# Kernel tuning notes

Hardware: AMD Instinct MI355X
Metric: run time of the kernel (lower is better)

## Reference

```python
import jax, jax.numpy as jnp
import numpy as np

DIM = 256

def setup_inputs() -> dict:
    key = jax.random.key(0)
    k1, k2 = jax.random.split(key)
    X = jax.random.normal(k1, (4, 4096, DIM), dtype=jnp.float32)
    # fused QKV projection weight, stored as (dim, 3*dim) so y = X @ W + b
    W = jax.random.normal(k2, (DIM, 3 * DIM), dtype=jnp.float32) * (1.0 / np.sqrt(DIM))
    b = jnp.zeros((3 * DIM,), dtype=jnp.float32)
    return {"X": X, "W": W, "b": b}

def reference(X, W, b):
    dim = X.shape[-1]
    QKV = X @ W + b                      # [B, S, 3*dim]
    Q, K, V = jnp.split(QKV, 3, axis=-1)  # each [B, S, dim]
    scores = jnp.einsum('bqd,bkd->bqk', Q, K) / jnp.sqrt(jnp.float32(dim))
    weights = jax.nn.softmax(scores, axis=-1)  # [B, S, S]
    return jnp.einsum('bqk,bkd->bqd', weights, V)
```

## Files before the change

kernel.cpp:

```cpp
#include <hip/hip_runtime.h>
#include <hip/hip_bf16.h>
#include <hip/hip_fp16.h>

#define DIMD 256
#define SLEN 4096
#define KT 32

typedef __attribute__((ext_vector_type(8))) short short8;
typedef __attribute__((ext_vector_type(4))) short bf16x4;
typedef __attribute__((ext_vector_type(4))) float f32x4;
typedef unsigned int u32;

__device__ __forceinline__ ushort f2bf(float x) {
  union { float f; unsigned u; } v; v.f = x;
  unsigned r = v.u + 0x7fffu + ((v.u >> 16) & 1u);
  return (ushort)(r >> 16);
}

typedef __attribute__((address_space(1))) const u32 g_u32;
typedef __attribute__((address_space(3))) u32 l_u32;
__device__ __forceinline__ void gld_lds16(const void* g, void* l) {
  __builtin_amdgcn_global_load_lds((g_u32*)g, (l_u32*)l, 16, 0, 0);
}

__global__ __launch_bounds__(256) void wt_prep(const float* __restrict__ W,
                                               ushort* __restrict__ Wt) {
  __shared__ float T[32][257];
  const int t = threadIdx.x;
  const int n0 = blockIdx.x * 32;
#pragma unroll
  for (int pass = 0; pass < 8; ++pass) {
    const int k = pass * 32 + (t >> 3);
    const int c4 = (t & 7) * 4;
    const float4 f = *(const float4*)&W[(size_t)k * 768 + n0 + c4];
    T[c4 + 0][k] = f.x; T[c4 + 1][k] = f.y; T[c4 + 2][k] = f.z; T[c4 + 3][k] = f.w;
  }
  __syncthreads();
  const int n = t >> 3, kb = (t & 7) * 32;
#pragma unroll
  for (int j8 = 0; j8 < 4; ++j8) {
    short8 o;
#pragma unroll
    for (int j = 0; j < 8; ++j) o[j] = (short)f2bf(T[n][kb + j8 * 8 + j]);
    *(short8*)&Wt[(size_t)(n0 + n) * 256 + kb + j8 * 8] = o;
  }
}

__global__ __launch_bounds__(256, 2) void qkv_proj(const float* __restrict__ X,
                                                   const ushort* __restrict__ Wt,
                                                   const float* __restrict__ bias,
                                                   ushort* __restrict__ Qo,
                                                   ushort* __restrict__ Ko,
                                                   ushort* __restrict__ Vto) {
  __shared__ ushort Xs[128 * 36];
  __shared__ ushort Ws[256 * 36];
  const int tid = threadIdx.x;
  const int w = tid >> 6, lane = tid & 63;
  const int qa = lane & 15, hi = lane >> 4;
  const int m0 = blockIdx.x * 128;
  const int seg = blockIdx.y;
  const int n0 = seg * 256;

  f32x4 acc[2][16];
#pragma unroll
  for (int t = 0; t < 2; ++t)
#pragma unroll
    for (int dc = 0; dc < 16; ++dc) acc[t][dc] = (f32x4){0.f, 0.f, 0.f, 0.f};

  for (int k0 = 0; k0 < 256; k0 += 32) {
    __syncthreads();
#pragma unroll
    for (int pass = 0; pass < 4; ++pass) {
      const int row = pass * 32 + (tid >> 3);
      const int c = tid & 7;
      const float4 f = *(const float4*)&X[(size_t)(m0 + row) * 256 + k0 + c * 4];
      bf16x4 h = {(short)f2bf(f.x), (short)f2bf(f.y), (short)f2bf(f.z), (short)f2bf(f.w)};
      *(bf16x4*)&Xs[row * 36 + c * 4] = h;
    }
#pragma unroll
    for (int pass = 0; pass < 4; ++pass) {
      const int n = pass * 64 + (tid >> 2);
      const int c = (tid & 3) * 8;
      short8 v = *(const short8*)&Wt[(size_t)(n0 + n) * 256 + k0 + c];
      *(short8*)&Ws[n * 36 + c] = v;
    }
    __syncthreads();
    const short8 xf0 = *(const short8*)&Xs[(w * 32 + qa) * 36 + hi * 8];
    const short8 xf1 = *(const short8*)&Xs[(w * 32 + 16 + qa) * 36 + hi * 8];
    __builtin_amdgcn_s_setprio(1);
#pragma unroll
    for (int dc = 0; dc < 16; ++dc) {
      const short8 wf = *(const short8*)&Ws[(dc * 16 + qa) * 36 + hi * 8];
      acc[0][dc] = __builtin_amdgcn_mfma_f32_16x16x32_bf16(xf0, wf, acc[0][dc], 0, 0, 0);
      acc[1][dc] = __builtin_amdgcn_mfma_f32_16x16x32_bf16(xf1, wf, acc[1][dc], 0, 0, 0);
    }
    __builtin_amdgcn_s_setprio(0);
  }

  const float sc = (seg == 0) ? 0.0625f : 1.0f;
#pragma unroll
  for (int dc = 0; dc < 16; ++dc) {
    const int nn = dc * 16 + qa;
    const float bv = bias[n0 + nn];
#pragma unroll
    for (int t = 0; t < 2; ++t) {
#pragma unroll
      for (int r = 0; r < 4; ++r) {
        const int m = m0 + w * 32 + t * 16 + hi * 4 + r;
        const ushort h = f2bf((acc[t][dc][r] + bv) * sc);
        if (seg == 0)      Qo[(size_t)m * 256 + nn] = h;
        else if (seg == 1) Ko[(size_t)m * 256 + nn] = h;
        else {
          const int bi = m >> 12, s = m & 4095;
          const int sp = (s & ~31) | ((s & 3) | (((s >> 4) & 1) << 2) | (((s >> 2) & 3) << 3));
          Vto[((size_t)bi * 256 + nn) * 4096 + sp] = h;
        }
      }
    }
  }
}

__device__ __forceinline__ void stage_kv(ushort* KsB, ushort* VsB,
                                         const ushort* Kb, const ushort* Vtb,
                                         int kv0, int w, int lane) {
#pragma unroll
  for (int it = 0; it < 2; ++it) {
    const int row = w * 4 + it * 2 + (lane >> 5);
    const int cb = (lane & 31) * 16;
    const char* src = (const char*)Kb + (size_t)(kv0 + row) * 512 + (cb ^ ((row & 7) << 4));
    gld_lds16(src, (char*)KsB + w * 2048 + it * 1024);
  }
#pragma unroll
  for (int it = 0; it < 2; ++it) {
    const int d = w * 32 + it * 16 + (lane >> 2);
    const int cb = (lane & 3) * 16;
    const char* src = (const char*)Vtb + (size_t)d * 8192 + (size_t)kv0 * 2 + (cb ^ ((d & 3) << 4));
    gld_lds16(src, (char*)VsB + w * 2048 + it * 1024);
  }
}

__global__ __launch_bounds__(512, 2) void flash_attn(const ushort* __restrict__ Q,
                                                     const ushort* __restrict__ K,
                                                     const ushort* __restrict__ Vt,
                                                     float* __restrict__ Out,
                                                     __half* __restrict__ Op,
                                                     float* __restrict__ Mp,
                                                     int nsplit, int kvn) {
  __shared__ __attribute__((aligned(16))) ushort Ks[3][KT * DIMD];
  __shared__ __attribute__((aligned(16))) ushort Vs[3][DIMD * KT];

  const int tid = threadIdx.x;
  const int w = tid >> 6, lane = tid & 63;
  const int nwg = gridDim.x;
  const int wg = (blockIdx.x & 7) * (nwg >> 3) + (blockIdx.x >> 3);
  const int split = wg >> 6;
  const int rest = wg & 63;
  const int b = rest >> 4;
  const int q0 = (rest & 15) * 256;
  const int qa = lane & 15, hi = lane >> 4;

  const ushort* Qr0 = Q + (size_t)(b * SLEN + q0 + w * 32 + qa) * DIMD;
  short8 qf0[8], qf1[8];
#pragma unroll
  for (int dc = 0; dc < 8; ++dc) {
    qf0[dc] = *(const short8*)(Qr0 + dc * 32 + hi * 8);
    qf1[dc] = *(const short8*)(Qr0 + 16 * DIMD + dc * 32 + hi * 8);
  }

  const f32x4 zero = {0.f, 0.f, 0.f, 0.f};
  f32x4 acc[2][16];
#pragma unroll
  for (int t = 0; t < 2; ++t)
#pragma unroll
    for (int dc = 0; dc < 16; ++dc) acc[t][dc] = zero;
  float mold0 = -1e30f, lrun0 = 0.f, mold1 = -1e30f, lrun1 = 0.f;
  short8 af0, af1;
  f32x4 sa0, sa1, sb0, sb1;

  const ushort* Kb = K + (size_t)b * SLEN * DIMD;
  const ushort* Vtb = Vt + (size_t)b * DIMD * SLEN;
  const int kv_begin = split * kvn;
  const int nt = kvn / KT;

  auto QK = [&](const char* KsB) {
    sa0 = zero; sa1 = zero; sb0 = zero; sb1 = zero;
    __builtin_amdgcn_s_setprio(1);
#pragma unroll
    for (int dc = 0; dc < 8; ++dc) {
      const int cb = dc * 64 + hi * 16;
      const short8 kf0 = *(const short8*)(KsB + ((qa * 512 + cb) ^ ((qa & 7) << 4)));
      const short8 kf1 = *(const short8*)(KsB + (((qa + 16) * 512 + cb) ^ ((qa & 7) << 4)));
      sa0 = __builtin_amdgcn_mfma_f32_16x16x32_bf16(kf0, qf0[dc], sa0, 0, 0, 0);
      sa1 = __builtin_amdgcn_mfma_f32_16x16x32_bf16(kf1, qf0[dc], sa1, 0, 0, 0);
      sb0 = __builtin_amdgcn_mfma_f32_16x16x32_bf16(kf0, qf1[dc], sb0, 0, 0, 0);
      sb1 = __builtin_amdgcn_mfma_f32_16x16x32_bf16(kf1, qf1[dc], sb1, 0, 0, 0);
    }
    __builtin_amdgcn_s_setprio(0);
  };

  auto FUSED = [&](const char* VsB, const char* KsB) {
    sa0 = zero; sa1 = zero; sb0 = zero; sb1 = zero;
    __builtin_amdgcn_s_setprio(1);
#pragma unroll
    for (int j = 0; j < 8; ++j) {
      const int d0 = (2 * j) * 16 + qa;
      const short8 vfa = *(const short8*)(VsB + d0 * 64 + ((hi * 16) ^ ((d0 & 3) << 4)));
      acc[0][2 * j] = __builtin_amdgcn_mfma_f32_16x16x32_bf16(af0, vfa, acc[0][2 * j], 0, 0, 0);
      acc[1][2 * j] = __builtin_amdgcn_mfma_f32_16x16x32_bf16(af1, vfa, acc[1][2 * j], 0, 0, 0);
      const int d1 = d0 + 16;
      const short8 vfb = *(const short8*)(VsB + d1 * 64 + ((hi * 16) ^ ((d1 & 3) << 4)));
      acc[0][2 * j + 1] = __builtin_amdgcn_mfma_f32_16x16x32_bf16(af0, vfb, acc[0][2 * j + 1], 0, 0, 0);
      acc[1][2 * j + 1] = __builtin_amdgcn_mfma_f32_16x16x32_bf16(af1, vfb, acc[1][2 * j + 1], 0, 0, 0);
      const int cb = j * 64 + hi * 16;
      const short8 kf0 = *(const short8*)(KsB + ((qa * 512 + cb) ^ ((qa & 7) << 4)));
      const short8 kf1 = *(const short8*)(KsB + (((qa + 16) * 512 + cb) ^ ((qa & 7) << 4)));
      sa0 = __builtin_amdgcn_mfma_f32_16x16x32_bf16(kf0, qf0[j], sa0, 0, 0, 0);
      sa1 = __builtin_amdgcn_mfma_f32_16x16x32_bf16(kf1, qf0[j], sa1, 0, 0, 0);
      sb0 = __builtin_amdgcn_mfma_f32_16x16x32_bf16(kf0, qf1[j], sb0, 0, 0, 0);
      sb1 = __builtin_amdgcn_mfma_f32_16x16x32_bf16(kf1, qf1[j], sb1, 0, 0, 0);
    }
    __builtin_amdgcn_s_setprio(0);
  };

  auto SM = [&]() {
    float m8a = fmaxf(fmaxf(fmaxf(sa0[0], sa0[1]), fmaxf(sa0[2], sa0[3])),
                      fmaxf(fmaxf(sa1[0], sa1[1]), fmaxf(sa1[2], sa1[3])));
    float m8b = fmaxf(fmaxf(fmaxf(sb0[0], sb0[1]), fmaxf(sb0[2], sb0[3])),
                      fmaxf(fmaxf(sb1[0], sb1[1]), fmaxf(sb1[2], sb1[3])));
    if (!__all(fmaxf(m8a - mold0, m8b - mold1) <= 4.0f)) {
      m8a = fmaxf(m8a, __shfl_xor(m8a, 16)); m8a = fmaxf(m8a, __shfl_xor(m8a, 32));
      m8b = fmaxf(m8b, __shfl_xor(m8b, 16)); m8b = fmaxf(m8b, __shfl_xor(m8b, 32));
      const float mn0 = fmaxf(mold0, m8a), fr0 = __expf(mold0 - mn0);
      const float mn1 = fmaxf(mold1, m8b), fr1 = __expf(mold1 - mn1);
      mold0 = mn0; lrun0 *= fr0; mold1 = mn1; lrun1 *= fr1;
      float fA[4], fB[4];
#pragma unroll
      for (int r = 0; r < 4; ++r) { fA[r] = __shfl(fr0, hi * 4 + r); fB[r] = __shfl(fr1, hi * 4 + r); }
#pragma unroll
      for (int dc = 0; dc < 16; ++dc)
#pragma unroll
        for (int r = 0; r < 4; ++r) { acc[0][dc][r] *= fA[r]; acc[1][dc][r] *= fB[r]; }
    }
    float ls0 = 0.f, ls1 = 0.f;
#pragma unroll
    for (int r = 0; r < 4; ++r) {
      float p = __expf(sa0[r] - mold0); ls0 += p; af0[r] = (short)f2bf(p);
      p = __expf(sa1[r] - mold0); ls0 += p; af0[4 + r] = (short)f2bf(p);
      p = __expf(sb0[r] - mold1); ls1 += p; af1[r] = (short)f2bf(p);
      p = __expf(sb1[r] - mold1); ls1 += p; af1[4 + r] = (short)f2bf(p);
    }
    lrun0 += ls0;
    lrun1 += ls1;
  };

  auto PV = [&](const char* VsB) {
    __builtin_amdgcn_s_setprio(1);
#pragma unroll
    for (int dc = 0; dc < 16; ++dc) {
      const int d = dc * 16 + qa;
      const short8 vf = *(const short8*)(VsB + d * 64 + ((hi * 16) ^ ((d & 3) << 4)));
      acc[0][dc] = __builtin_amdgcn_mfma_f32_16x16x32_bf16(af0, vf, acc[0][dc], 0, 0, 0);
      acc[1][dc] = __builtin_amdgcn_mfma_f32_16x16x32_bf16(af1, vf, acc[1][dc], 0, 0, 0);
    }
    __builtin_amdgcn_s_setprio(0);
  };

  stage_kv(Ks[0], Vs[0], Kb, Vtb, kv_begin, w, lane);
  stage_kv(Ks[1], Vs[1], Kb, Vtb, kv_begin + KT, w, lane);
  asm volatile("s_waitcnt vmcnt(0)" ::: "memory");
  __builtin_amdgcn_s_barrier();
  __builtin_amdgcn_sched_barrier(0);
  QK((const char*)Ks[0]);
  SM();

  int cur = 0;
  for (int it = 0; it < nt - 2; ++it) {
    const int nb = (cur == 0) ? 2 : cur - 1;
    stage_kv(Ks[nb], Vs[nb], Kb, Vtb, kv_begin + (it + 2) * KT, w, lane);
    __builtin_amdgcn_sched_barrier(0);
    asm volatile("s_waitcnt vmcnt(4)" ::: "memory");
    __builtin_amdgcn_sched_barrier(0);
    const int nx = (cur == 2) ? 0 : cur + 1;
    FUSED((const char*)Vs[cur], (const char*)Ks[nx]);
    SM();
    __builtin_amdgcn_s_barrier();
    __builtin_amdgcn_sched_barrier(0);
    cur = nx;
  }
  asm volatile("s_waitcnt vmcnt(0)" ::: "memory");
  __builtin_amdgcn_s_barrier();
  __builtin_amdgcn_sched_barrier(0);
  {
    const int nx = (cur == 2) ? 0 : cur + 1;
    FUSED((const char*)Vs[cur], (const char*)Ks[nx]);
    SM();
    PV((const char*)Vs[nx]);
  }

  lrun0 += __shfl_xor(lrun0, 16); lrun0 += __shfl_xor(lrun0, 32);
  lrun1 += __shfl_xor(lrun1, 16); lrun1 += __shfl_xor(lrun1, 32);
  float inv0[4], inv1[4];
#pragma unroll
  for (int r = 0; r < 4; ++r) {
    inv0[r] = 1.f / __shfl(lrun0, hi * 4 + r);
    inv1[r] = 1.f / __shfl(lrun1, hi * 4 + r);
  }
  if (nsplit == 1) {
    float* Ob = Out + (size_t)(b * SLEN + q0 + w * 32) * DIMD;
#pragma unroll
    for (int dc = 0; dc < 16; ++dc)
#pragma unroll
      for (int r = 0; r < 4; ++r) {
        Ob[(size_t)(hi * 4 + r) * DIMD + dc * 16 + qa] = acc[0][dc][r] * inv0[r];
        Ob[(size_t)(16 + hi * 4 + r) * DIMD + dc * 16 + qa] = acc[1][dc][r] * inv1[r];
      }
  } else {
    const size_t qrow0 = (size_t)b * SLEN + q0 + w * 32;
#pragma unroll
    for (int dc = 0; dc < 16; ++dc)
#pragma unroll
      for (int r = 0; r < 4; ++r) {
        Op[((qrow0 + hi * 4 + r) * nsplit + split) * DIMD + dc * 16 + qa] =
            __float2half(acc[0][dc][r] * inv0[r]);
        Op[((qrow0 + 16 + hi * 4 + r) * nsplit + split) * DIMD + dc * 16 + qa] =
            __float2half(acc[1][dc][r] * inv1[r]);
      }
    if (hi == 0) {
      Mp[(qrow0 + qa) * nsplit + split] = mold0 + __logf(lrun0);
      Mp[(qrow0 + 16 + qa) * nsplit + split] = mold1 + __logf(lrun1);
    }
  }
}

__global__ __launch_bounds__(256) void attn_merge(const __half* __restrict__ Op,
                                                  const float* __restrict__ Mp,
                                                  float* __restrict__ Out, int nsplit) {
  const int q = blockIdx.x, d = threadIdx.x;
  float Mx = -1e30f;
  for (int i = 0; i < nsplit; ++i) Mx = fmaxf(Mx, Mp[(size_t)q * nsplit + i]);
  float Wsum = 0.f, o = 0.f;
  for (int i = 0; i < nsplit; ++i) {
    const float wgt = __expf(Mp[(size_t)q * nsplit + i] - Mx);
    Wsum += wgt;
    o += wgt * __half2float(Op[((size_t)q * nsplit + i) * DIMD + d]);
  }
  Out[(size_t)q * DIMD + d] = o / Wsum;
}

extern "C" void kernel_launch(void* const* d_in, const int* in_sizes, int n_in,
                              void* d_out, int out_size, void* d_ws, size_t ws_size,
                              hipStream_t stream) {
  const float* X = (const float*)d_in[0];
  const float* W = (const float*)d_in[1];
  const float* bias = (const float*)d_in[2];
  char* wsb = (char*)d_ws;
  ushort* qw = (ushort*)wsb;
  ushort* kw = qw + (size_t)16384 * 256;
  ushort* vtw = kw + (size_t)16384 * 256;
  ushort* wt = vtw + (size_t)16384 * 256;
  const size_t head_bytes = (size_t)3 * 16384 * 256 * 2 + 768 * 256 * 2;
  const size_t per_split = (size_t)16384 * 256 * 2 + (size_t)16384 * 4;
  int nsplit = 1;
  if (ws_size >= head_bytes + 4 * per_split)      nsplit = 4;
  else if (ws_size >= head_bytes + 2 * per_split) nsplit = 2;
  __half* Op = (__half*)(wsb + head_bytes);
  float* Mp = (float*)(wsb + head_bytes + (size_t)nsplit * 16384 * 256 * 2);

  wt_prep<<<dim3(24), 256, 0, stream>>>(W, wt);
  qkv_proj<<<dim3(128, 3), 256, 0, stream>>>(X, wt, bias, qw, kw, vtw);
  flash_attn<<<dim3(64 * nsplit), 512, 0, stream>>>(qw, kw, vtw, (float*)d_out,
                                                    Op, Mp, nsplit, 4096 / nsplit);
  if (nsplit > 1)
    attn_merge<<<dim3(16384), 256, 0, stream>>>(Op, Mp, (float*)d_out, nsplit);
}
```

Before: 142.4 us.

## Pre-convert X to bf16 and double-buffer QKV projection with direct global-to-LDS loads

Adds an x_prep kernel that converts X to bf16 once, so the three qkv_proj segments no longer each re-read fp32 X and convert it in-loop. The projection's K-loop now stages tiles into double-buffered LDS via global_load_lds with an XOR swizzle instead of padded rows, prefetching the next tile while MFMAs run on the current one. This costs an extra kernel launch, an extra bf16 copy of X in the workspace, and a larger head region that may lower nsplit for smaller workspaces.

```diff
diff --git a/kernel.cpp b/kernel.cpp
--- a/kernel.cpp
+++ b/kernel.cpp
@@ -21,6 +21,16 @@
 typedef __attribute__((address_space(3))) u32 l_u32;
 __device__ __forceinline__ void gld_lds16(const void* g, void* l) {
   __builtin_amdgcn_global_load_lds((g_u32*)g, (l_u32*)l, 16, 0, 0);
+}
+
+__global__ __launch_bounds__(256) void x_prep(const float* __restrict__ X,
+                                              ushort* __restrict__ Xb) {
+  const size_t i = ((size_t)blockIdx.x * 256 + threadIdx.x) * 8;
+  const float4 a = *(const float4*)&X[i];
+  const float4 b = *(const float4*)&X[i + 4];
+  short8 o = {(short)f2bf(a.x), (short)f2bf(a.y), (short)f2bf(a.z), (short)f2bf(a.w),
+              (short)f2bf(b.x), (short)f2bf(b.y), (short)f2bf(b.z), (short)f2bf(b.w)};
+  *(short8*)&Xb[i] = o;
 }
 
 __global__ __launch_bounds__(256) void wt_prep(const float* __restrict__ W,
@@ -46,14 +56,33 @@
   }
 }
 
-__global__ __launch_bounds__(256, 2) void qkv_proj(const float* __restrict__ X,
+__device__ __forceinline__ void stage_xw(ushort* XsB, ushort* WsB,
+                                         const ushort* Xbm, const ushort* Wtn,
+                                         int k0, int w, int lane) {
+#pragma unroll
+  for (int it = 0; it < 2; ++it) {
+    const int row = w * 32 + it * 16 + (lane >> 2);
+    const int cb = (lane & 3) * 16;
+    const char* src = (const char*)Xbm + (size_t)row * 512 + (size_t)k0 * 2 + (cb ^ ((row & 3) << 4));
+    gld_lds16(src, (char*)XsB + w * 2048 + it * 1024);
+  }
+#pragma unroll
+  for (int it = 0; it < 4; ++it) {
+    const int row = w * 64 + it * 16 + (lane >> 2);
+    const int cb = (lane & 3) * 16;
+    const char* src = (const char*)Wtn + (size_t)row * 512 + (size_t)k0 * 2 + (cb ^ ((row & 3) << 4));
+    gld_lds16(src, (char*)WsB + w * 4096 + it * 1024);
+  }
+}
+
+__global__ __launch_bounds__(256, 2) void qkv_proj(const ushort* __restrict__ Xb,
                                                    const ushort* __restrict__ Wt,
                                                    const float* __restrict__ bias,
                                                    ushort* __restrict__ Qo,
                                                    ushort* __restrict__ Ko,
                                                    ushort* __restrict__ Vto) {
-  __shared__ ushort Xs[128 * 36];
-  __shared__ ushort Ws[256 * 36];
+  __shared__ __attribute__((aligned(16))) ushort Xs[2][128 * 32];
+  __shared__ __attribute__((aligned(16))) ushort Ws[2][256 * 32];
   const int tid = threadIdx.x;
   const int w = tid >> 6, lane = tid & 63;
   const int qa = lane & 15, hi = lane >> 4;
@@ -67,34 +96,36 @@
 #pragma unroll
     for (int dc = 0; dc < 16; ++dc) acc[t][dc] = (f32x4){0.f, 0.f, 0.f, 0.f};
 
+  const ushort* Xbm = Xb + (size_t)m0 * 256;
+  const ushort* Wtn = Wt + (size_t)n0 * 256;
+
+  stage_xw(Xs[0], Ws[0], Xbm, Wtn, 0, w, lane);
+  asm volatile("s_waitcnt vmcnt(0)" ::: "memory");
+  __builtin_amdgcn_s_barrier();
+  __builtin_amdgcn_sched_barrier(0);
+
   for (int k0 = 0; k0 < 256; k0 += 32) {
-    __syncthreads();
-#pragma unroll
-    for (int pass = 0; pass < 4; ++pass) {
-      const int row = pass * 32 + (tid >> 3);
-      const int c = tid & 7;
-      const float4 f = *(const float4*)&X[(size_t)(m0 + row) * 256 + k0 + c * 4];
-      bf16x4 h = {(short)f2bf(f.x), (short)f2bf(f.y), (short)f2bf(f.z), (short)f2bf(f.w)};
-      *(bf16x4*)&Xs[row * 36 + c * 4] = h;
-    }
-#pragma unroll
-    for (int pass = 0; pass < 4; ++pass) {
-      const int n = pass * 64 + (tid >> 2);
-      const int c = (tid & 3) * 8;
-      short8 v = *(const short8*)&Wt[(size_t)(n0 + n) * 256 + k0 + c];
-      *(short8*)&Ws[n * 36 + c] = v;
-    }
-    __syncthreads();
-    const short8 xf0 = *(const short8*)&Xs[(w * 32 + qa) * 36 + hi * 8];
-    const short8 xf1 = *(const short8*)&Xs[(w * 32 + 16 + qa) * 36 + hi * 8];
+    const int buf = (k0 >> 5) & 1;
+    if (k0 < 224)
+      stage_xw(Xs[buf ^ 1], Ws[buf ^ 1], Xbm, Wtn, k0 + 32, w, lane);
+    __builtin_amdgcn_sched_barrier(0);
+    const char* XsB = (const char*)Xs[buf];
+    const char* WsB = (const char*)Ws[buf];
+    const int r0 = w * 32 + qa;
+    const int xsw = (hi * 16) ^ ((r0 & 3) << 4);
+    const short8 xf0 = *(const short8*)(XsB + r0 * 64 + xsw);
+    const short8 xf1 = *(const short8*)(XsB + (r0 + 16) * 64 + xsw);
     __builtin_amdgcn_s_setprio(1);
 #pragma unroll
     for (int dc = 0; dc < 16; ++dc) {
-      const short8 wf = *(const short8*)&Ws[(dc * 16 + qa) * 36 + hi * 8];
+      const short8 wf = *(const short8*)(WsB + (dc * 16 + qa) * 64 + ((hi * 16) ^ ((qa & 3) << 4)));
       acc[0][dc] = __builtin_amdgcn_mfma_f32_16x16x32_bf16(xf0, wf, acc[0][dc], 0, 0, 0);
       acc[1][dc] = __builtin_amdgcn_mfma_f32_16x16x32_bf16(xf1, wf, acc[1][dc], 0, 0, 0);
     }
     __builtin_amdgcn_s_setprio(0);
+    asm volatile("s_waitcnt vmcnt(0)" ::: "memory");
+    __builtin_amdgcn_s_barrier();
+    __builtin_amdgcn_sched_barrier(0);
   }
 
   const float sc = (seg == 0) ? 0.0625f : 1.0f;
@@ -358,7 +389,8 @@
   ushort* kw = qw + (size_t)16384 * 256;
   ushort* vtw = kw + (size_t)16384 * 256;
   ushort* wt = vtw + (size_t)16384 * 256;
-  const size_t head_bytes = (size_t)3 * 16384 * 256 * 2 + 768 * 256 * 2;
+  ushort* xb = wt + (size_t)768 * 256;
+  const size_t head_bytes = (size_t)4 * 16384 * 256 * 2 + 768 * 256 * 2;
   const size_t per_split = (size_t)16384 * 256 * 2 + (size_t)16384 * 4;
   int nsplit = 1;
   if (ws_size >= head_bytes + 4 * per_split)      nsplit = 4;
@@ -366,8 +398,9 @@
   __half* Op = (__half*)(wsb + head_bytes);
   float* Mp = (float*)(wsb + head_bytes + (size_t)nsplit * 16384 * 256 * 2);
 
+  x_prep<<<dim3(2048), 256, 0, stream>>>(X, xb);
   wt_prep<<<dim3(24), 256, 0, stream>>>(W, wt);
-  qkv_proj<<<dim3(128, 3), 256, 0, stream>>>(X, wt, bias, qw, kw, vtw);
+  qkv_proj<<<dim3(128, 3), 256, 0, stream>>>(xb, wt, bias, qw, kw, vtw);
   flash_attn<<<dim3(64 * nsplit), 512, 0, stream>>>(qw, kw, vtw, (float*)d_out,
                                                     Op, Mp, nsplit, 4096 / nsplit);
   if (nsplit > 1)
```

After: 143.4 us. About the same (+0.7%).
